# Optimization experiments

Measured on AMD Instinct MI355X. Metric: run time of the kernel, lower is better.

The kernel has to match this reference:

```python
import jax, jax.numpy as jnp
import numpy as np

OUTCOMES = [8, 8, 8, 8, 8, 8]           # concept outcome counts (concepts_order)
N_TOTAL = int(np.prod(OUTCOMES))        # 262144 joint states
N_VALID = 8192                          # admissible states
B, D = 4096, 1024


def setup_inputs() -> dict:
    key = jax.random.key(0)
    k1, k2 = jax.random.split(key)
    embeddings = jax.random.normal(k1, (B, D), dtype=jnp.float32)
    W = jax.random.normal(k2, (N_VALID, D), dtype=jnp.float32) * 0.02
    b = jnp.zeros((N_VALID,), dtype=jnp.float32)
    # unique sorted admissible-state indices, like torch.argwhere(mask)
    rng = np.random.default_rng(0)
    valid_states = jnp.asarray(
        np.sort(rng.choice(N_TOTAL, size=N_VALID, replace=False)).astype(np.int32))
    return {"embeddings": embeddings, "W": W, "b": b, "valid_states": valid_states}


def reference(embeddings, W, b, valid_states):
    # softmax over valid states: [B, N_VALID]
    probs = jax.nn.softmax(embeddings @ W.T + b, axis=1)
    probs_t = probs.T  # [N_VALID, B] for leading-axis segment reduction
    marginals = []
    stride = N_TOTAL
    for n_i in OUTCOMES:
        stride //= n_i
        # digit of each valid joint-state index along this concept's axis
        digit = (valid_states // stride) % n_i  # [N_VALID]
        # equivalent to scattering probs into the full joint tensor and
        # summing over all other concept axes, without materializing it
        m = jax.ops.segment_sum(probs_t, digit, num_segments=n_i).T  # [B, n_i]
        marginals.append(m)
    return jnp.stack(marginals)  # [n_concepts, B, 8]
```

## Files before the change

kernel.cpp:

```cpp
#include <hip/hip_runtime.h>
#include <hip/hip_bf16.h>
#include <cstdint>
#include <cstddef>

typedef __bf16 bf16_t;
typedef bf16_t bf16x8 __attribute__((ext_vector_type(8)));
typedef bf16_t bf16x4 __attribute__((ext_vector_type(4)));
typedef float  f32x4  __attribute__((ext_vector_type(4)));
typedef unsigned int u32;

#define BROWS 4096
#define NV    8192
#define KD    1024
#define KSPLIT 16
#define NT    16

#define GLL(gsrc, ldst) \
  __builtin_amdgcn_global_load_lds((const __attribute__((address_space(1))) u32*)(gsrc), \
                                   (__attribute__((address_space(3))) u32*)(ldst), 16, 0, 0)
#define FENCE asm volatile("" ::: "memory")

__global__ void cvt_kernel(const float* __restrict__ src, bf16_t* __restrict__ dst, int n4) {
  int idx = blockIdx.x * blockDim.x + threadIdx.x;
  int stride = gridDim.x * blockDim.x;
  for (int i = idx; i < n4; i += stride) {
    float4 v = ((const float4*)src)[i];
    bf16x4 o;
    o[0] = (bf16_t)v.x; o[1] = (bf16_t)v.y; o[2] = (bf16_t)v.z; o[3] = (bf16_t)v.w;
    ((bf16x4*)dst)[i] = o;
  }
}

__global__ void build_st_kernel(const int* __restrict__ vstate, bf16_t* __restrict__ st) {
  int g = blockIdx.x * blockDim.x + threadIdx.x;
  if (g >= 48 * NV) return;
  int bucket = g >> 13;
  int j = g & (NV - 1);
  int c = bucket >> 3;
  int d = bucket & 7;
  int dig = (vstate[j] >> (15 - 3 * c)) & 7;
  st[g] = (bf16_t)(dig == d ? 1.0f : 0.0f);
}

__global__ __launch_bounds__(512, 2)
void gemm_exp_kernel(const bf16_t* __restrict__ A, const bf16_t* __restrict__ B,
                     const float* __restrict__ bias, bf16_t* __restrict__ expout) {
  __shared__ __align__(16) char lds[2][65536];
  #define AKH0 0
  #define AKH1 16384
  #define BKH0 32768
  #define BKH1 49152

  const int t    = threadIdx.x;
  const int lane = t & 63;
  const int wv   = t >> 6;
  const int wm   = wv >> 2;
  const int wn   = wv & 3;
  const int fr   = lane & 15;
  const int fq   = lane >> 4;

  int bid = blockIdx.x;
  int wg  = (bid & 7) * 64 + (bid >> 3);
  const int mt = wg >> 5;
  const int nt = wg & 31;
  const int row0 = mt * 256;
  const int col0 = nt * 256;

  const int srow = lane >> 2;
  const int skel = ((lane & 3) ^ ((lane >> 3) & 3)) * 8;
  const bf16_t* aptr = A + (size_t)(row0 + wv * 32 + srow) * KD + skel;
  const bf16_t* bptr = B + (size_t)(col0 + wv * 32 + srow) * KD + skel;
  const int dchunk = (wv * 2) * 1024;

  const int xsw = (fr & 6) << 3;
  const int base_a = (((wm * 128 + fr) * 64 + fq * 16) ^ xsw);
  const int base_b = 32768 + (((wn * 64 + fr) * 64 + fq * 16) ^ xsw);

  f32x4 acc[8][4] = {};

  GLL(aptr, &lds[0][AKH0 + dchunk]);
  GLL(aptr + 16 * KD, &lds[0][AKH0 + dchunk + 1024]);
  GLL(bptr, &lds[0][BKH0 + dchunk]);
  GLL(bptr + 16 * KD, &lds[0][BKH0 + dchunk + 1024]);
  GLL(aptr + 32, &lds[0][AKH1 + dchunk]);
  GLL(aptr + 32 + 16 * KD, &lds[0][AKH1 + dchunk + 1024]);
  GLL(bptr + 32, &lds[0][BKH1 + dchunk]);
  GLL(bptr + 32 + 16 * KD, &lds[0][BKH1 + dchunk + 1024]);
  asm volatile("s_waitcnt vmcnt(4)" ::: "memory");
  __builtin_amdgcn_s_barrier();
  FENCE;

  int cur = 0;
  for (int kt = 0; kt < NT; ++kt) {
    const char* bufp = lds[cur];
    char* nbuf = lds[cur ^ 1];
    const bf16_t* anext = aptr + (kt + 1) * 64;
    const bf16_t* bnext = bptr + (kt + 1) * 64;
    const bool pf = (kt + 1 < NT);

    bf16x8 bfrag[4], af[4];

#pragma unroll
    for (int n = 0; n < 4; ++n)
      bfrag[n] = *(const bf16x8*)(bufp + base_b + n * 1024);
#pragma unroll
    for (int mi = 0; mi < 4; ++mi)
      af[mi] = *(const bf16x8*)(bufp + base_a + mi * 1024);
    if (pf) {
      GLL(anext, &nbuf[AKH0 + dchunk]);
      GLL(anext + 16 * KD, &nbuf[AKH0 + dchunk + 1024]);
    }
    FENCE; __builtin_amdgcn_s_barrier(); FENCE;
    __builtin_amdgcn_s_setprio(1);
#pragma unroll
    for (int mi = 0; mi < 4; ++mi)
#pragma unroll
      for (int n = 0; n < 4; ++n)
        acc[mi][n] = __builtin_amdgcn_mfma_f32_16x16x32_bf16(af[mi], bfrag[n], acc[mi][n], 0, 0, 0);
    __builtin_amdgcn_s_setprio(0);
    FENCE; __builtin_amdgcn_s_barrier(); FENCE;

#pragma unroll
    for (int mi = 0; mi < 4; ++mi)
      af[mi] = *(const bf16x8*)(bufp + base_a + (4 + mi) * 1024);
    if (pf) {
      GLL(bnext, &nbuf[BKH0 + dchunk]);
      GLL(bnext + 16 * KD, &nbuf[BKH0 + dchunk + 1024]);
    }
    FENCE; __builtin_amdgcn_s_barrier(); FENCE;
    __builtin_amdgcn_s_setprio(1);
#pragma unroll
    for (int mi = 0; mi < 4; ++mi)
#pragma unroll
      for (int n = 0; n < 4; ++n)
        acc[4 + mi][n] = __builtin_amdgcn_mfma_f32_16x16x32_bf16(af[mi], bfrag[n], acc[4 + mi][n], 0, 0, 0);
    __builtin_amdgcn_s_setprio(0);
    if (pf) asm volatile("s_waitcnt vmcnt(4)" ::: "memory");
    else    asm volatile("s_waitcnt vmcnt(0)" ::: "memory");
    FENCE; __builtin_amdgcn_s_barrier(); FENCE;

#pragma unroll
    for (int n = 0; n < 4; ++n)
      bfrag[n] = *(const bf16x8*)(bufp + base_b + 16384 + n * 1024);
#pragma unroll
    for (int mi = 0; mi < 4; ++mi)
      af[mi] = *(const bf16x8*)(bufp + base_a + 16384 + mi * 1024);
    if (pf) {
      GLL(anext + 32, &nbuf[AKH1 + dchunk]);
      GLL(anext + 32 + 16 * KD, &nbuf[AKH1 + dchunk + 1024]);
    }
    FENCE; __builtin_amdgcn_s_barrier(); FENCE;
    __builtin_amdgcn_s_setprio(1);
#pragma unroll
    for (int mi = 0; mi < 4; ++mi)
#pragma unroll
      for (int n = 0; n < 4; ++n)
        acc[mi][n] = __builtin_amdgcn_mfma_f32_16x16x32_bf16(af[mi], bfrag[n], acc[mi][n], 0, 0, 0);
    __builtin_amdgcn_s_setprio(0);
    FENCE; __builtin_amdgcn_s_barrier(); FENCE;

#pragma unroll
    for (int mi = 0; mi < 4; ++mi)
      af[mi] = *(const bf16x8*)(bufp + base_a + 16384 + (4 + mi) * 1024);
    if (pf) {
      GLL(bnext + 32, &nbuf[BKH1 + dchunk]);
      GLL(bnext + 32 + 16 * KD, &nbuf[BKH1 + dchunk + 1024]);
    }
    FENCE; __builtin_amdgcn_s_barrier(); FENCE;
    __builtin_amdgcn_s_setprio(1);
#pragma unroll
    for (int mi = 0; mi < 4; ++mi)
#pragma unroll
      for (int n = 0; n < 4; ++n)
        acc[4 + mi][n] = __builtin_amdgcn_mfma_f32_16x16x32_bf16(af[mi], bfrag[n], acc[4 + mi][n], 0, 0, 0);
    __builtin_amdgcn_s_setprio(0);
    if (pf) asm volatile("s_waitcnt vmcnt(4)" ::: "memory");
    FENCE; __builtin_amdgcn_s_barrier(); FENCE;

    cur ^= 1;
  }

#pragma unroll
  for (int n = 0; n < 4; ++n) {
    const int col = col0 + wn * 64 + n * 16 + fr;
    const float bb = bias[col];
#pragma unroll
    for (int m = 0; m < 8; ++m) {
      const int rowb = row0 + wm * 128 + m * 16 + fq * 4;
#pragma unroll
      for (int r = 0; r < 4; ++r) {
        float e = exp2f((acc[m][n][r] + bb) * 1.44269504088896340736f);
        expout[(size_t)(rowb + r) * NV + col] = (bf16_t)e;
      }
    }
  }
}

__global__ __launch_bounds__(256)
void marginal_mfma_kernel(const bf16_t* __restrict__ expbuf, const bf16_t* __restrict__ st,
                          float* __restrict__ part) {
  __shared__ bf16_t sE[128][32];
  __shared__ bf16_t sS[48][32];

  const int t    = threadIdx.x;
  const int lane = t & 63;
  const int wv   = t >> 6;

  const int rt = blockIdx.x >> 4;
  const int ks = blockIdx.x & (KSPLIT - 1);
  const int row0 = rt * 128;
  const int kbase = ks * (NV / KSPLIT);

  const int srow = t >> 2;
  const int skel = (t & 3) * 8;
  const bf16_t* ep0 = expbuf + (size_t)(row0 + srow) * NV + kbase + skel;
  const bf16_t* ep1 = ep0 + (size_t)64 * NV;
  const bf16_t* sp0 = st + (size_t)srow * NV + kbase + skel;
  bf16_t* se0 = &sE[0][0] + (wv * 64) * 8;
  bf16_t* se1 = &sE[0][0] + (256 + wv * 64) * 8;
  bf16_t* ss0 = &sS[0][0] + (wv * 64) * 8;

  const int fr = lane & 15;
  const int fq = lane >> 4;

  f32x4 acc[2][3] = {};

  for (int kk = 0; kk < NV / KSPLIT; kk += 32) {
    GLL(ep0 + kk, se0);
    GLL(ep1 + kk, se1);
    if (wv < 3) GLL(sp0 + kk, ss0);
    __syncthreads();

    bf16x8 af[2], bg[3];
#pragma unroll
    for (int m = 0; m < 2; ++m)
      af[m] = *(const bf16x8*)&sE[wv * 32 + m * 16 + fr][fq * 8];
#pragma unroll
    for (int n = 0; n < 3; ++n)
      bg[n] = *(const bf16x8*)&sS[n * 16 + fr][fq * 8];
#pragma unroll
    for (int m = 0; m < 2; ++m)
#pragma unroll
      for (int n = 0; n < 3; ++n)
        acc[m][n] = __builtin_amdgcn_mfma_f32_16x16x32_bf16(af[m], bg[n], acc[m][n], 0, 0, 0);
    __syncthreads();
  }

  float* pbase = part + (size_t)ks * BROWS * 48;
#pragma unroll
  for (int m = 0; m < 2; ++m) {
    const int rowb = row0 + wv * 32 + m * 16 + fq * 4;
#pragma unroll
    for (int n = 0; n < 3; ++n) {
      const int bucket = n * 16 + fr;
#pragma unroll
      for (int r = 0; r < 4; ++r)
        pbase[(size_t)(rowb + r) * 48 + bucket] = acc[m][n][r];
    }
  }
}

__global__ __launch_bounds__(64)
void reduce_kernel(const float* __restrict__ part, float* __restrict__ out) {
  const int b = blockIdx.x;
  const int t = threadIdx.x;
  __shared__ float fin[48];
  if (t < 48) {
    float s = 0.f;
#pragma unroll
    for (int ks = 0; ks < KSPLIT; ++ks)
      s += part[((size_t)ks * BROWS + b) * 48 + t];
    fin[t] = s;
  }
  __syncthreads();
  if (t < 48) {
    float total = fin[0] + fin[1] + fin[2] + fin[3] + fin[4] + fin[5] + fin[6] + fin[7];
    out[(size_t)(t >> 3) * BROWS * 8 + (size_t)b * 8 + (t & 7)] = fin[t] / total;
  }
}

extern "C" void kernel_launch(void* const* d_in, const int* in_sizes, int n_in,
                              void* d_out, int out_size, void* d_ws, size_t ws_size,
                              hipStream_t stream) {
  const float* E    = (const float*)d_in[0];
  const float* W    = (const float*)d_in[1];
  const float* bias = (const float*)d_in[2];
  const int*   vs   = (const int*)d_in[3];
  float* out = (float*)d_out;

  char* ws = (char*)d_ws;
  size_t off = 0;
  bf16_t* Eb     = (bf16_t*)(ws + off); off += (size_t)BROWS * KD * 2;
  bf16_t* Wb     = (bf16_t*)(ws + off); off += (size_t)NV * KD * 2;
  bf16_t* expbuf = (bf16_t*)(ws + off); off += (size_t)BROWS * NV * 2;
  bf16_t* st     = (bf16_t*)(ws + off); off += (size_t)48 * NV * 2;
  float*  part   = (float*)(ws + off);  off += (size_t)KSPLIT * BROWS * 48 * 4;

  build_st_kernel<<<(48 * NV + 255) / 256, 256, 0, stream>>>(vs, st);
  cvt_kernel<<<2048, 256, 0, stream>>>(E, Eb, BROWS * KD / 4);
  cvt_kernel<<<2048, 256, 0, stream>>>(W, Wb, NV * KD / 4);
  gemm_exp_kernel<<<512, 512, 0, stream>>>(Eb, Wb, bias, expbuf);
  marginal_mfma_kernel<<<32 * KSPLIT, 256, 0, stream>>>(expbuf, st, part);
  reduce_kernel<<<BROWS, 64, 0, stream>>>(part, out);
}
```

Baseline: 122.4 us.

## Collapse GEMM main loop to one barrier per k-tile with full-tile register loads

Replaces the four-phase interleaved schedule, which had many barriers and staggered global-to-LDS prefetches, with a simpler loop. Each iteration loads the whole k-tile's A and B fragments from LDS into registers, issues all eight prefetch loads for the next tile at once, runs 64 MFMAs, then waits on vmcnt(0) and takes a single barrier. This cuts barrier and synchronisation overhead, but raises register pressure and waits for the whole prefetch at the end of every iteration.

```diff
diff --git a/kernel.cpp b/kernel.cpp
--- a/kernel.cpp
+++ b/kernel.cpp
@@ -86,7 +86,7 @@
   GLL(aptr + 32 + 16 * KD, &lds[0][AKH1 + dchunk + 1024]);
   GLL(bptr + 32, &lds[0][BKH1 + dchunk]);
   GLL(bptr + 32 + 16 * KD, &lds[0][BKH1 + dchunk + 1024]);
-  asm volatile("s_waitcnt vmcnt(4)" ::: "memory");
+  asm volatile("s_waitcnt vmcnt(0)" ::: "memory");
   __builtin_amdgcn_s_barrier();
   FENCE;
 
@@ -94,89 +94,54 @@
   for (int kt = 0; kt < NT; ++kt) {
     const char* bufp = lds[cur];
     char* nbuf = lds[cur ^ 1];
-    const bf16_t* anext = aptr + (kt + 1) * 64;
-    const bf16_t* bnext = bptr + (kt + 1) * 64;
     const bool pf = (kt + 1 < NT);
 
-    bf16x8 bfrag[4], af[4];
+    bf16x8 a0[8], b0[4], a1[8], b1[4];
 
 #pragma unroll
     for (int n = 0; n < 4; ++n)
-      bfrag[n] = *(const bf16x8*)(bufp + base_b + n * 1024);
-#pragma unroll
-    for (int mi = 0; mi < 4; ++mi)
-      af[mi] = *(const bf16x8*)(bufp + base_a + mi * 1024);
+      b0[n] = *(const bf16x8*)(bufp + base_b + n * 1024);
+#pragma unroll
+    for (int m = 0; m < 8; ++m)
+      a0[m] = *(const bf16x8*)(bufp + base_a + m * 1024);
+
     if (pf) {
-      GLL(anext, &nbuf[AKH0 + dchunk]);
-      GLL(anext + 16 * KD, &nbuf[AKH0 + dchunk + 1024]);
+      const bf16_t* an = aptr + (kt + 1) * 64;
+      const bf16_t* bn = bptr + (kt + 1) * 64;
+      GLL(an, &nbuf[AKH0 + dchunk]);
+      GLL(an + 16 * KD, &nbuf[AKH0 + dchunk + 1024]);
+      GLL(bn, &nbuf[BKH0 + dchunk]);
+      GLL(bn + 16 * KD, &nbuf[BKH0 + dchunk + 1024]);
+      GLL(an + 32, &nbuf[AKH1 + dchunk]);
+      GLL(an + 32 + 16 * KD, &nbuf[AKH1 + dchunk + 1024]);
+      GLL(bn + 32, &nbuf[BKH1 + dchunk]);
+      GLL(bn + 32 + 16 * KD, &nbuf[BKH1 + dchunk + 1024]);
     }
-    FENCE; __builtin_amdgcn_s_barrier(); FENCE;
+
+#pragma unroll
+    for (int n = 0; n < 4; ++n)
+      b1[n] = *(const bf16x8*)(bufp + base_b + 16384 + n * 1024);
+#pragma unroll
+    for (int m = 0; m < 8; ++m)
+      a1[m] = *(const bf16x8*)(bufp + base_a + 16384 + m * 1024);
+
     __builtin_amdgcn_s_setprio(1);
 #pragma unroll
-    for (int mi = 0; mi < 4; ++mi)
+    for (int m = 0; m < 8; ++m)
 #pragma unroll
       for (int n = 0; n < 4; ++n)
-        acc[mi][n] = __builtin_amdgcn_mfma_f32_16x16x32_bf16(af[mi], bfrag[n], acc[mi][n], 0, 0, 0);
+        acc[m][n] = __builtin_amdgcn_mfma_f32_16x16x32_bf16(a0[m], b0[n], acc[m][n], 0, 0, 0);
+#pragma unroll
+    for (int m = 0; m < 8; ++m)
+#pragma unroll
+      for (int n = 0; n < 4; ++n)
+        acc[m][n] = __builtin_amdgcn_mfma_f32_16x16x32_bf16(a1[m], b1[n], acc[m][n], 0, 0, 0);
     __builtin_amdgcn_s_setprio(0);
-    FENCE; __builtin_amdgcn_s_barrier(); FENCE;
-
-#pragma unroll
-    for (int mi = 0; mi < 4; ++mi)
-      af[mi] = *(const bf16x8*)(bufp + base_a + (4 + mi) * 1024);
-    if (pf) {
-      GLL(bnext, &nbuf[BKH0 + dchunk]);
-      GLL(bnext + 16 * KD, &nbuf[BKH0 + dchunk + 1024]);
-    }
-    FENCE; __builtin_amdgcn_s_barrier(); FENCE;
-    __builtin_amdgcn_s_setprio(1);
-#pragma unroll
-    for (int mi = 0; mi < 4; ++mi)
-#pragma unroll
-      for (int n = 0; n < 4; ++n)
-        acc[4 + mi][n] = __builtin_amdgcn_mfma_f32_16x16x32_bf16(af[mi], bfrag[n], acc[4 + mi][n], 0, 0, 0);
-    __builtin_amdgcn_s_setprio(0);
-    if (pf) asm volatile("s_waitcnt vmcnt(4)" ::: "memory");
-    else    asm volatile("s_waitcnt vmcnt(0)" ::: "memory");
-    FENCE; __builtin_amdgcn_s_barrier(); FENCE;
-
-#pragma unroll
-    for (int n = 0; n < 4; ++n)
-      bfrag[n] = *(const bf16x8*)(bufp + base_b + 16384 + n * 1024);
-#pragma unroll
-    for (int mi = 0; mi < 4; ++mi)
-      af[mi] = *(const bf16x8*)(bufp + base_a + 16384 + mi * 1024);
-    if (pf) {
-      GLL(anext + 32, &nbuf[AKH1 + dchunk]);
-      GLL(anext + 32 + 16 * KD, &nbuf[AKH1 + dchunk + 1024]);
-    }
-    FENCE; __builtin_amdgcn_s_barrier(); FENCE;
-    __builtin_amdgcn_s_setprio(1);
-#pragma unroll
-    for (int mi = 0; mi < 4; ++mi)
-#pragma unroll
-      for (int n = 0; n < 4; ++n)
-        acc[mi][n] = __builtin_amdgcn_mfma_f32_16x16x32_bf16(af[mi], bfrag[n], acc[mi][n], 0, 0, 0);
-    __builtin_amdgcn_s_setprio(0);
-    FENCE; __builtin_amdgcn_s_barrier(); FENCE;
-
-#pragma unroll
-    for (int mi = 0; mi < 4; ++mi)
-      af[mi] = *(const bf16x8*)(bufp + base_a + 16384 + (4 + mi) * 1024);
-    if (pf) {
-      GLL(bnext + 32, &nbuf[BKH1 + dchunk]);
-      GLL(bnext + 32 + 16 * KD, &nbuf[BKH1 + dchunk + 1024]);
-    }
-    FENCE; __builtin_amdgcn_s_barrier(); FENCE;
-    __builtin_amdgcn_s_setprio(1);
-#pragma unroll
-    for (int mi = 0; mi < 4; ++mi)
-#pragma unroll
-      for (int n = 0; n < 4; ++n)
-        acc[4 + mi][n] = __builtin_amdgcn_mfma_f32_16x16x32_bf16(af[mi], bfrag[n], acc[4 + mi][n], 0, 0, 0);
-    __builtin_amdgcn_s_setprio(0);
-    if (pf) asm volatile("s_waitcnt vmcnt(4)" ::: "memory");
-    FENCE; __builtin_amdgcn_s_barrier(); FENCE;
-
+
+    asm volatile("s_waitcnt vmcnt(0)" ::: "memory");
+    __builtin_amdgcn_sched_barrier(0);
+    __builtin_amdgcn_s_barrier();
+    FENCE;
     cur ^= 1;
   }
 
```

New measurement: 119.6 us. -2.3%, faster.
